# Kernel tuning notes

Measured on AMD Instinct MI355X. Metric: run time of the kernel, lower is better.

Reference implementation:

```python
import jax, jax.numpy as jnp
import numpy as np

WINDOW_SIZE = 11
SIGMA = 1.5
C1 = 0.01 ** 2
C2 = 0.03 ** 2


def _gaussian_window(window_size, sigma, channel, dtype=jnp.float32):
    x = np.arange(window_size) - window_size // 2
    g = np.exp(-(x.astype(np.float64) ** 2) / (2.0 * sigma ** 2))
    g = (g / g.sum()).astype(np.float32)
    w2d = np.outer(g, g)  # [K, K]
    # depthwise kernel: [C, 1, K, K] (OIHW with feature_group_count=C)
    w = np.broadcast_to(w2d, (channel, 1, window_size, window_size))
    return jnp.asarray(w, dtype=dtype)


def _dw_conv(x, window):
    # x: [B, C, H, W]; window: [C, 1, K, K]; SAME padding via pad=K//2 (K odd)
    k = window.shape[-1]
    p = k // 2
    return jax.lax.conv_general_dilated(
        x, window,
        window_strides=(1, 1),
        padding=((p, p), (p, p)),
        dimension_numbers=("NCHW", "OIHW", "NCHW"),
        feature_group_count=x.shape[1],
    )


def setup_inputs() -> dict:
    key = jax.random.key(0)
    k1, k2 = jax.random.split(key)
    shape = (32, 3, 512, 512)
    img1 = jax.random.uniform(k1, shape, dtype=jnp.float32)
    img2 = jax.random.uniform(k2, shape, dtype=jnp.float32)
    return {"img1": img1, "img2": img2}


def reference(img1, img2):
    channel = img1.shape[1]
    window = _gaussian_window(WINDOW_SIZE, SIGMA, channel, img1.dtype)

    mu1 = _dw_conv(img1, window)
    mu2 = _dw_conv(img2, window)
    mu1_sq = mu1 * mu1
    mu2_sq = mu2 * mu2
    mu1_mu2 = mu1 * mu2

    sigma1_sq = _dw_conv(img1 * img1, window) - mu1_sq
    sigma2_sq = _dw_conv(img2 * img2, window) - mu2_sq
    sigma12 = _dw_conv(img1 * img2, window) - mu1_mu2

    ssim_map = ((2.0 * mu1_mu2 + C1) * (2.0 * sigma12 + C2)) / (
        (mu1_sq + mu2_sq + C1) * (sigma1_sq + sigma2_sq + C2)
    )
    return 1.0 - jnp.mean(ssim_map)
```

## Files before the change

### kernel.cpp

```cpp
#include <hip/hip_runtime.h>

#define HH 512
#define WW 512
#define PLANES 96
#define RSTRIP 32
#define NPIX 25165824.0f

#define G0 0.2660117f
#define G1 0.2130056f
#define G2 0.1093607f
#define G3 0.0360008f
#define G4 0.0075988f
#define G5 0.0010284f

#define C1F 1e-4f
#define C2F 9e-4f

typedef float v2f __attribute__((ext_vector_type(2)));
#define PKFMA(a, b, c) __builtin_elementwise_fma(a, b, c)

#define DECL_HIST2(Z) v2f Z##0={0,0},Z##1={0,0},Z##2={0,0},Z##3={0,0},Z##4={0,0},\
                          Z##5={0,0},Z##6={0,0},Z##7={0,0},Z##8={0,0},Z##9={0,0},Z##10={0,0}
#define SHIFT_HIST(Z) do{Z##0=Z##1;Z##1=Z##2;Z##2=Z##3;Z##3=Z##4;Z##4=Z##5;\
                         Z##5=Z##6;Z##6=Z##7;Z##7=Z##8;Z##8=Z##9;Z##9=Z##10;}while(0)
#define VCONV2(Z) PKFMA(g5, Z##0+Z##10, PKFMA(g4, Z##1+Z##9, PKFMA(g3, Z##2+Z##8,\
                  PKFMA(g2, Z##3+Z##7, PKFMA(g1, Z##4+Z##6, g0*Z##5)))))

__global__ __launch_bounds__(256) __attribute__((amdgpu_waves_per_eu(6, 8)))
void ssim_main(const float* __restrict__ img1,
               const float* __restrict__ img2,
               float* __restrict__ acc) {
    __shared__ v2f luv[2][272];
    const int tid = threadIdx.x;
    const int c0  = blockIdx.x * 256;
    const int r0  = blockIdx.y * RSTRIP;
    const int p   = blockIdx.z;
    const size_t pb = (size_t)p * (HH * WW);

    const int cs = c0 - 5 + tid;
    const bool in_main = (unsigned)cs < (unsigned)WW;
    const bool halo    = tid < 10;
    const bool in_halo = halo && (unsigned)(cs + 256) < (unsigned)WW;

    const float* rx = img1 + pb + (ptrdiff_t)(r0 - 5) * WW + cs;
    const float* ry = img2 + pb + (ptrdiff_t)(r0 - 5) * WW + cs;

    const v2f g0 = {G0, G0}, g1 = {G1, G1}, g2 = {G2, G2},
              g3 = {G3, G3}, g4 = {G4, G4}, g5 = {G5, G5};

    DECL_HIST2(AB); DECL_HIST2(PQ);

    float lsum = 0.f;

#pragma unroll 2
    for (int t = r0 - 5; t <= r0 + RSTRIP + 4; ++t, rx += WW, ry += WW) {
        SHIFT_HIST(AB); SHIFT_HIST(PQ);

        v2f nAB = {0.f, 0.f}, nPQ = {0.f, 0.f};
        if ((unsigned)t < (unsigned)HH) {
            const int buf = t & 1;
            float sx = 0.f, sy = 0.f, hx = 0.f, hy = 0.f;
            if (in_main) { sx = rx[0];   sy = ry[0];   }
            if (in_halo) { hx = rx[256]; hy = ry[256]; }
            luv[buf][tid] = v2f{sx + sy, sx - sy};
            if (halo) luv[buf][tid + 256] = v2f{hx + hy, hx - hy};
            __syncthreads();

            const v2f* w = &luv[buf][tid];
            {
                const v2f uv5 = w[5];
                nAB = g0 * uv5;
                nPQ = g0 * (uv5 * uv5);
            }
#define HPAIR(KL, KR, GK) { \
            const v2f l = w[KL], r = w[KR]; \
            nAB = PKFMA(GK, l + r, nAB); \
            nPQ = PKFMA(GK, PKFMA(l, l, r * r), nPQ); }
            HPAIR(4, 6, g1) HPAIR(3, 7, g2) HPAIR(2, 8, g3)
            HPAIR(1, 9, g4) HPAIR(0, 10, g5)
#undef HPAIR
        }
        AB10 = nAB; PQ10 = nPQ;

        const int s = t - 5 - r0;
        if ((unsigned)s < (unsigned)RSTRIP) {
            const v2f mu = VCONV2(AB);
            const v2f c2 = VCONV2(PQ);
            const float a = mu.x * mu.x;
            const float b = mu.y * mu.y;
            const float musq = 0.5f  * (a + b);
            const float mu12 = 0.25f * (a - b);
            const float csq  = 0.5f  * (c2.x + c2.y);
            const float cxy  = 0.25f * (c2.x - c2.y);
            const float ssum = csq - musq;
            const float s12  = cxy - mu12;
            const float num = fmaf(2.f, mu12, C1F) * fmaf(2.f, s12, C2F);
            const float den = (musq + C1F) * (ssum + C2F);
            lsum += num * __builtin_amdgcn_rcpf(den);
        }
    }

#pragma unroll
    for (int off = 32; off > 0; off >>= 1)
        lsum += __shfl_down(lsum, off, 64);
    __shared__ float ws4[4];
    const int lane = threadIdx.x & 63;
    const int wv   = threadIdx.x >> 6;
    if (lane == 0) ws4[wv] = lsum;
    __syncthreads();
    if (threadIdx.x == 0)
        atomicAdd(acc, ws4[0] + ws4[1] + ws4[2] + ws4[3]);
}

__global__ void ssim_zero(float* acc) { acc[0] = 0.f; }

__global__ void ssim_finalize(const float* __restrict__ acc, float* __restrict__ out) {
    out[0] = 1.f - acc[0] * (1.f / NPIX);
}

extern "C" void kernel_launch(void* const* d_in, const int* in_sizes, int n_in,
                              void* d_out, int out_size, void* d_ws, size_t ws_size,
                              hipStream_t stream) {
    const float* img1 = (const float*)d_in[0];
    const float* img2 = (const float*)d_in[1];
    float* out = (float*)d_out;
    float* acc = (float*)d_ws;

    ssim_zero<<<1, 1, 0, stream>>>(acc);
    dim3 grid(WW / 256, HH / RSTRIP, PLANES);
    ssim_main<<<grid, 256, 0, stream>>>(img1, img2, acc);
    ssim_finalize<<<1, 1, 0, stream>>>(acc, out);
}
```

Measured before the change: 272.4 us.

## Use per-wave LDS tiles with wave barriers and prefetch next row

Each wavefront now owns a 64-column tile plus its own 10-column halo in shared memory, so the block-wide __syncthreads per row becomes a wave-level barrier. Global loads for the next row are issued one iteration early into registers to overlap memory latency with the horizontal convolution. The cost is more halo loads, since every 64 columns now re-read 10 halo columns instead of every 256, plus extra registers for the prefetch and a larger unroll.

Result: no change. 273.4 us (+0.3%).

```diff
diff --git a/kernel.cpp b/kernel.cpp
--- a/kernel.cpp
+++ b/kernel.cpp
@@ -30,17 +30,19 @@
 void ssim_main(const float* __restrict__ img1,
                const float* __restrict__ img2,
                float* __restrict__ acc) {
-    __shared__ v2f luv[2][272];
-    const int tid = threadIdx.x;
-    const int c0  = blockIdx.x * 256;
-    const int r0  = blockIdx.y * RSTRIP;
-    const int p   = blockIdx.z;
+    __shared__ v2f luv[2][4][80];
+    const int tid  = threadIdx.x;
+    const int lane = tid & 63;
+    const int wv   = tid >> 6;
+    const int base = blockIdx.x * 256 + wv * 64;
+    const int r0   = blockIdx.y * RSTRIP;
+    const int p    = blockIdx.z;
     const size_t pb = (size_t)p * (HH * WW);
 
-    const int cs = c0 - 5 + tid;
+    const int cs = base - 5 + lane;
     const bool in_main = (unsigned)cs < (unsigned)WW;
-    const bool halo    = tid < 10;
-    const bool in_halo = halo && (unsigned)(cs + 256) < (unsigned)WW;
+    const bool halo    = lane < 10;
+    const bool in_halo = halo && (unsigned)(cs + 64) < (unsigned)WW;
 
     const float* rx = img1 + pb + (ptrdiff_t)(r0 - 5) * WW + cs;
     const float* ry = img2 + pb + (ptrdiff_t)(r0 - 5) * WW + cs;
@@ -50,36 +52,51 @@
 
     DECL_HIST2(AB); DECL_HIST2(PQ);
 
+    float cx = 0.f, cy = 0.f, chx = 0.f, chy = 0.f;
+    if ((unsigned)(r0 - 5) < (unsigned)HH) {
+        if (in_main) { cx  = rx[0];  cy  = ry[0];  }
+        if (in_halo) { chx = rx[64]; chy = ry[64]; }
+    }
+
     float lsum = 0.f;
+    const int tend = r0 + RSTRIP + 4;
 
-#pragma unroll 2
-    for (int t = r0 - 5; t <= r0 + RSTRIP + 4; ++t, rx += WW, ry += WW) {
+#pragma unroll 6
+    for (int t = r0 - 5; t <= tend; ++t, rx += WW, ry += WW) {
         SHIFT_HIST(AB); SHIFT_HIST(PQ);
+
+        float nx2 = 0.f, ny2 = 0.f, nhx = 0.f, nhy = 0.f;
+        const int tn = t + 1;
+        if (tn <= tend && (unsigned)tn < (unsigned)HH) {
+            if (in_main) { nx2 = rx[WW];      ny2 = ry[WW];      }
+            if (in_halo) { nhx = rx[WW + 64]; nhy = ry[WW + 64]; }
+        }
 
         v2f nAB = {0.f, 0.f}, nPQ = {0.f, 0.f};
         if ((unsigned)t < (unsigned)HH) {
-            const int buf = t & 1;
-            float sx = 0.f, sy = 0.f, hx = 0.f, hy = 0.f;
-            if (in_main) { sx = rx[0];   sy = ry[0];   }
-            if (in_halo) { hx = rx[256]; hy = ry[256]; }
-            luv[buf][tid] = v2f{sx + sy, sx - sy};
-            if (halo) luv[buf][tid + 256] = v2f{hx + hy, hx - hy};
-            __syncthreads();
+            v2f* sb = &luv[t & 1][wv][0];
+            sb[lane] = v2f{cx + cy, cx - cy};
+            if (halo) sb[64 + lane] = v2f{chx + chy, chx - chy};
+            __asm__ volatile("" ::: "memory");
+            __builtin_amdgcn_wave_barrier();
 
-            const v2f* w = &luv[buf][tid];
+            const v2f* wp = sb + lane;
             {
-                const v2f uv5 = w[5];
+                const v2f uv5 = wp[5];
                 nAB = g0 * uv5;
                 nPQ = g0 * (uv5 * uv5);
             }
 #define HPAIR(KL, KR, GK) { \
-            const v2f l = w[KL], r = w[KR]; \
+            const v2f l = wp[KL], r = wp[KR]; \
             nAB = PKFMA(GK, l + r, nAB); \
             nPQ = PKFMA(GK, PKFMA(l, l, r * r), nPQ); }
             HPAIR(4, 6, g1) HPAIR(3, 7, g2) HPAIR(2, 8, g3)
             HPAIR(1, 9, g4) HPAIR(0, 10, g5)
 #undef HPAIR
+            __asm__ volatile("" ::: "memory");
+            __builtin_amdgcn_wave_barrier();
         }
+        cx = nx2; cy = ny2; chx = nhx; chy = nhy;
         AB10 = nAB; PQ10 = nPQ;
 
         const int s = t - 5 - r0;
@@ -104,8 +121,6 @@
     for (int off = 32; off > 0; off >>= 1)
         lsum += __shfl_down(lsum, off, 64);
     __shared__ float ws4[4];
-    const int lane = threadIdx.x & 63;
-    const int wv   = threadIdx.x >> 6;
     if (lane == 0) ws4[wv] = lsum;
     __syncthreads();
     if (threadIdx.x == 0)
```
